# Performance work log

Measured on AMD Instinct MI355X. Metric: run time of the kernel, lower is better.

## Reference

```python
import jax, jax.numpy as jnp
import numpy as np

B, N, M = 8, 1024, 64          # graphs, ops/graph, machines/graph
OPF, MF = 16, 8                # raw feature dims
H, D, L = 8, 64, 3             # heads, head dim, HGT layers
F = H * D                      # 512 = hidden_dim * num_heads
KC = 8                         # compatible machines per op
NOP, NM = B * N, B * M
EPS = 1e-5


def _graph_ln(x, w, b):
    # PyG LayerNorm(mode='graph') with batch=None: scalar mean/std over the whole tensor
    x = x - x.mean()
    return x / (x.std() + EPS) * w + b


def _seg_softmax(a, idx, n):
    amax = jax.ops.segment_max(a, idx, num_segments=n)
    amax = jnp.where(jnp.isfinite(amax), amax, 0.0)
    ex = jnp.exp(a - amax[idx])
    s = jax.ops.segment_sum(ex, idx, num_segments=n)
    return ex / (s[idx] + 1e-16)


def _forward(op_x, machine_x, W_emb_op, b_emb_op, W_emb_m, b_emb_m,
             opn_w, opn_b, mn_w, mn_b, Wk, bk, Wq, bq, Wv, bv,
             A_rel, M_rel, p_rel, W_out, b_out, skip, ln_w, ln_b,
             ei_precedes, ei_canproc, ei_compat):
    x_op = _graph_ln(op_x @ W_emb_op + b_emb_op, opn_w, opn_b)
    x_m = _graph_ln(machine_x @ W_emb_m + b_emb_m, mn_w, mn_b)
    s0, d0 = ei_precedes   # op -> op
    s1, d1 = ei_canproc    # machine -> op
    s2, d2 = ei_compat     # op -> machine
    scale = 1.0 / jnp.sqrt(jnp.float32(D))
    for l in range(L):
        k_op = (x_op @ Wk[l, 0] + bk[l, 0]).reshape(NOP, H, D)
        q_op = (x_op @ Wq[l, 0] + bq[l, 0]).reshape(NOP, H, D)
        v_op = (x_op @ Wv[l, 0] + bv[l, 0]).reshape(NOP, H, D)
        k_m = (x_m @ Wk[l, 1] + bk[l, 1]).reshape(NM, H, D)
        q_m = (x_m @ Wq[l, 1] + bq[l, 1]).reshape(NM, H, D)
        v_m = (x_m @ Wv[l, 1] + bv[l, 1]).reshape(NM, H, D)
        # relation-specific per-head transforms (a_rel/m_rel of HGTConv)
        k0 = jnp.einsum('nhd,hde->nhe', k_op, A_rel[l, 0]); v0 = jnp.einsum('nhd,hde->nhe', v_op, M_rel[l, 0])
        k1 = jnp.einsum('nhd,hde->nhe', k_m, A_rel[l, 1]);  v1 = jnp.einsum('nhd,hde->nhe', v_m, M_rel[l, 1])
        k2 = jnp.einsum('nhd,hde->nhe', k_op, A_rel[l, 2]); v2 = jnp.einsum('nhd,hde->nhe', v_op, M_rel[l, 2])
        # attention into op nodes: joint softmax over both incoming edge types
        a0 = (q_op[d0] * k0[s0]).sum(-1) * p_rel[l, 0] * scale   # [E0,H]
        a1 = (q_op[d1] * k1[s1]).sum(-1) * p_rel[l, 1] * scale   # [E1,H]
        a_op = jnp.concatenate([a0, a1]); dd = jnp.concatenate([d0, d1])
        w = _seg_softmax(a_op, dd, NOP)
        msg = jnp.concatenate([v0[s0], v1[s1]]) * w[:, :, None]
        agg_op = jax.ops.segment_sum(msg, dd, num_segments=NOP).reshape(NOP, F)
        # attention into machine nodes
        a2 = (q_m[d2] * k2[s2]).sum(-1) * p_rel[l, 2] * scale
        w2 = _seg_softmax(a2, d2, NM)
        agg_m = jax.ops.segment_sum(v2[s2] * w2[:, :, None], d2, num_segments=NM).reshape(NM, F)
        # output projection + learned skip gate (HGTConv internals)
        o_op = jax.nn.gelu(agg_op, approximate=False) @ W_out[l, 0] + b_out[l, 0]
        o_m = jax.nn.gelu(agg_m, approximate=False) @ W_out[l, 1] + b_out[l, 1]
        g_op = jax.nn.sigmoid(skip[l, 0]); g_m = jax.nn.sigmoid(skip[l, 1])
        o_op = g_op * o_op + (1.0 - g_op) * x_op
        o_m = g_m * o_m + (1.0 - g_m) * x_m
        # wrapper residual + dropout(eval=identity) + graph layer norm
        x_op = _graph_ln(o_op + x_op, ln_w[l], ln_b[l])
        x_m = _graph_ln(o_m + x_m, ln_w[l], ln_b[l])
    fea_j = x_op.reshape(B, N, F)
    fea_m = x_m.reshape(B, M, F)
    return fea_j, fea_m, fea_j.mean(1, keepdims=True), fea_m.mean(1, keepdims=True)


def setup_inputs() -> dict:
    key = jax.random.key(0)
    ks = jax.random.split(key, 12)
    rng = np.random.default_rng(0)
    ids = np.arange(NOP).reshape(B, N)
    src0 = ids[:, :-1].ravel(); dst0 = ids[:, 1:].ravel()
    mach = rng.integers(0, M, size=(B, N, KC)) + (np.arange(B) * M)[:, None, None]
    ops = np.broadcast_to(ids[:, :, None], (B, N, KC))
    ei_precedes = jnp.asarray(np.stack([src0, dst0]), dtype=jnp.int32)
    ei_canproc = jnp.asarray(np.stack([mach.ravel(), ops.ravel()]), dtype=jnp.int32)
    ei_compat = jnp.asarray(np.stack([ops.ravel(), mach.ravel()]), dtype=jnp.int32)
    n = lambda k, sh, s=0.05: jax.random.normal(k, sh, dtype=jnp.float32) * s
    return dict(
        op_x=n(ks[0], (NOP, OPF), 1.0),
        machine_x=n(ks[1], (NM, MF), 1.0),
        W_emb_op=n(ks[2], (OPF, F)), b_emb_op=jnp.zeros((F,), jnp.float32),
        W_emb_m=n(ks[3], (MF, F)), b_emb_m=jnp.zeros((F,), jnp.float32),
        opn_w=jnp.ones((F,), jnp.float32), opn_b=jnp.zeros((F,), jnp.float32),
        mn_w=jnp.ones((F,), jnp.float32), mn_b=jnp.zeros((F,), jnp.float32),
        Wk=n(ks[4], (L, 2, F, F)), bk=jnp.zeros((L, 2, F), jnp.float32),
        Wq=n(ks[5], (L, 2, F, F)), bq=jnp.zeros((L, 2, F), jnp.float32),
        Wv=n(ks[6], (L, 2, F, F)), bv=jnp.zeros((L, 2, F), jnp.float32),
        A_rel=n(ks[7], (L, 3, H, D, D)), M_rel=n(ks[8], (L, 3, H, D, D)),
        p_rel=jnp.ones((L, 3, H), jnp.float32),
        W_out=n(ks[9], (L, 2, F, F)), b_out=jnp.zeros((L, 2, F), jnp.float32),
        skip=jnp.ones((L, 2), jnp.float32),
        ln_w=jnp.ones((L, F), jnp.float32), ln_b=jnp.zeros((L, F), jnp.float32),
        ei_precedes=ei_precedes, ei_canproc=ei_canproc, ei_compat=ei_compat,
    )


def reference(op_x, machine_x, W_emb_op, b_emb_op, W_emb_m, b_emb_m,
              opn_w, opn_b, mn_w, mn_b, Wk, bk, Wq, bq, Wv, bv,
              A_rel, M_rel, p_rel, W_out, b_out, skip, ln_w, ln_b,
              ei_precedes, ei_canproc, ei_compat):
    return _forward(op_x, machine_x, W_emb_op, b_emb_op, W_emb_m, b_emb_m,
                    opn_w, opn_b, mn_w, mn_b, Wk, bk, Wq, bq, Wv, bv,
                    A_rel, M_rel, p_rel, W_out, b_out, skip, ln_w, ln_b,
                    ei_precedes, ei_canproc, ei_compat)
```

## Files before the change

### kernel.cpp

```cpp
#include <hip/hip_runtime.h>

typedef unsigned short u16;
typedef __attribute__((ext_vector_type(4))) float floatx4;
typedef __attribute__((ext_vector_type(8))) short shortx8;
typedef __attribute__((ext_vector_type(4))) short shortx4;

#define NOPS 8192
#define NMS  512
#define CQ   2560
#define CM   1536
#define TOPC (NOPS*512)
#define TMC  (NMS*512)

__device__ __forceinline__ float bf2f(u16 u){ return __uint_as_float(((unsigned)u)<<16); }
__device__ __forceinline__ u16 f2bf(float f){
  unsigned u = __float_as_uint(f);
  u += 0x7FFFu + ((u>>16)&1u);
  return (u16)(u>>16);
}
__device__ __forceinline__ float wred(float v){
  #pragma unroll
  for (int o=32;o;o>>=1) v += __shfl_xor(v,o,64);
  return v;
}
__device__ __forceinline__ float geluf(float x){
  return 0.5f*x*(1.f+erff(x*0.70710678118654752f));
}
__device__ __forceinline__ void block_stat_out2(float s, float s2, float* pstat, int slot){
  __shared__ float sb[8];
  s = wred(s); s2 = wred(s2);
  int wv = threadIdx.x >> 6;
  if ((threadIdx.x & 63) == 0){ sb[wv*2] = s; sb[wv*2+1] = s2; }
  __syncthreads();
  if (threadIdx.x == 0){
    float a = 0.f, b = 0.f;
    int nw = blockDim.x >> 6;
    for (int i=0;i<nw;++i){ a += sb[i*2]; b += sb[i*2+1]; }
    pstat[slot*2]   = a;
    pstat[slot*2+1] = b;
  }
}

__global__ __launch_bounds__(256) void cnt2_k(const int* __restrict__ s1, float* __restrict__ Ct,
                                              float* __restrict__ Cn){
  int idx = blockIdx.x*256 + threadIdx.x;
  int n = idx >> 6, l = idx & 63;
  const int* row = s1 + n*8;
  int cnt = 0;
  #pragma unroll
  for (int j=0;j<8;++j) cnt += ((row[j] & 63) == l);
  float f = (float)cnt;
  Cn[(size_t)n*64 + l] = f;
  int b = n >> 10, nl = n & 1023;
  Ct[(size_t)((b<<6) + l)*1024 + nl] = f;
}

__global__ __launch_bounds__(256) void tw_k(const float* __restrict__ Wout, const float* __restrict__ Wq,
                                            u16* __restrict__ Wout_t, u16* __restrict__ Wc_op_t,
                                            u16* __restrict__ Wc_m_t){
  __shared__ u16 t[64][65];
  int g = blockIdx.x;
  const float* s; u16* d;
  if (g < 6){
    s = Wout + (size_t)g*262144;
    d = Wout_t + (size_t)g*262144;
  } else {
    int blk = g - 6; int l = blk >> 1, side = blk & 1;
    s = Wq + (size_t)blk*262144;
    d = side ? (Wc_m_t + (size_t)l*CM*512) : (Wc_op_t + (size_t)l*CQ*512);
  }
  int kb = blockIdx.y*64, nb = blockIdx.z*64;
  int tx = threadIdx.x & 63, ty4 = threadIdx.x >> 6;
  #pragma unroll 4
  for (int p=0;p<16;++p){
    int k = ty4 + p*4;
    t[k][tx] = f2bf(s[(size_t)(kb+k)*512 + nb + tx]);
  }
  __syncthreads();
  #pragma unroll 4
  for (int p=0;p<16;++p){
    int n = ty4 + p*4;
    d[(size_t)(nb+n)*512 + kb + tx] = t[tx][n];
  }
}

__global__ void qb_k(const float* __restrict__ bq, float* bias_op, float* bias_m){
  int i = blockIdx.x*blockDim.x + threadIdx.x;
  if (i >= 3072) return;
  int l = i >> 10, side = (i >> 9) & 1, f = i & 511;
  float v = bq[(l*2+side)*512 + f];
  if (side==0) bias_op[l*CQ + f] = v; else bias_m[l*CM + f] = v;
}

__global__ __launch_bounds__(256) void combine3_k(const float* __restrict__ Wk, const float* __restrict__ Wv,
                                                  const float* __restrict__ Ar, const float* __restrict__ Mr,
                                                  u16* __restrict__ Wc_op_t, u16* __restrict__ Wc_m_t){
  __shared__ u16 As[64*72];
  __shared__ u16 Bs[128*72];
  int gx = blockIdx.x;
  int l = gx/48; int rem = gx - l*48; int s = rem >> 3; int h = rem & 7;
  int side = (s < 4) ? 0 : 1;
  int r = (s < 4) ? (s+1) : (s-3);
  int useK = side==0 ? (s==0 || s==2) : (s==4);
  int rel  = side==0 ? ((s<2)?0:2) : 1;
  const float* W   = (useK ? Wk : Wv) + (size_t)(l*2+side)*262144;
  const float* Rel = (useK ? Ar : Mr) + ((size_t)(l*3+rel)*8 + h)*4096;
  int h64 = h*64;
  u16* Wt = side ? (Wc_m_t + (size_t)l*CM*512) : (Wc_op_t + (size_t)l*CQ*512);
  int rbase = r*512 + h64;
  int cc0 = blockIdx.y * 128;
  int tid = threadIdx.x, lane = tid & 63, wave = tid >> 6;
  {
    int d = tid >> 2, e0 = (tid & 3) * 16;
    #pragma unroll
    for (int j=0;j<16;++j) As[(e0+j)*72 + d] = f2bf(Rel[d*64 + e0 + j]);
  }
  {
    int ccl = tid >> 1, d0 = (tid & 1) * 32;
    const float* src = W + (size_t)(cc0+ccl)*512 + h64 + d0;
    #pragma unroll
    for (int j=0;j<32;j+=4){
      floatx4 v = *(const floatx4*)(src + j);
      shortx4 sv;
      #pragma unroll
      for (int e=0;e<4;++e) sv[e] = (short)f2bf(v[e]);
      *(shortx4*)(Bs + ccl*72 + d0 + j) = sv;
    }
  }
  __syncthreads();
  int wm = wave & 1, wn = wave >> 1;
  int mrow = lane & 15, quad = lane >> 4;
  floatx4 acc[2][4];
  #pragma unroll
  for (int a=0;a<2;++a)
    #pragma unroll
    for (int b=0;b<4;++b) acc[a][b] = (floatx4){0.f,0.f,0.f,0.f};
  #pragma unroll
  for (int ks=0; ks<2; ++ks){
    shortx8 af[2], bf[4];
    #pragma unroll
    for (int mt=0;mt<2;++mt) af[mt] = *(const shortx8*)(As + (wm*32 + mt*16 + mrow)*72 + ks*32 + quad*8);
    #pragma unroll
    for (int nt=0;nt<4;++nt) bf[nt] = *(const shortx8*)(Bs + (wn*64 + nt*16 + mrow)*72 + ks*32 + quad*8);
    #pragma unroll
    for (int mt=0;mt<2;++mt)
      #pragma unroll
      for (int nt=0;nt<4;++nt)
        acc[mt][nt] = __builtin_amdgcn_mfma_f32_16x16x32_bf16(af[mt], bf[nt], acc[mt][nt], 0, 0, 0);
  }
  #pragma unroll
  for (int mt=0;mt<2;++mt){
    #pragma unroll
    for (int nt=0;nt<4;++nt){
      int ccl = wn*64 + nt*16 + mrow;
      #pragma unroll
      for (int r2=0;r2<4;++r2){
        int e = wm*32 + mt*16 + quad*4 + r2;
        Wt[(size_t)(rbase + e)*512 + cc0 + ccl] = f2bf(acc[mt][nt][r2]);
      }
    }
  }
}
__global__ void cbias_k(const float* __restrict__ bk, const float* __restrict__ bv,
                        const float* __restrict__ Ar, const float* __restrict__ Mr,
                        float* bias_op, float* bias_m){
  int gx = blockIdx.x; int e = threadIdx.x;
  int l = gx/48; int rem = gx - l*48; int s = rem >> 3; int h = rem & 7;
  int side = (s < 4) ? 0 : 1;
  int r = (s < 4) ? (s+1) : (s-3);
  int useK = side==0 ? (s==0 || s==2) : (s==4);
  int rel  = side==0 ? ((s<2)?0:2) : 1;
  const float* bb  = (useK ? bk : bv) + (size_t)(l*2+side)*512 + h*64;
  const float* Rel = (useK ? Ar : Mr) + ((size_t)(l*3+rel)*8 + h)*4096;
  float acc = 0.f;
  for (int d=0; d<64; ++d) acc += bb[d]*Rel[d*64 + e];
  float* bias = side ? (bias_m + l*CM) : (bias_op + l*CQ);
  bias[r*512 + h*64 + e] = acc;
}

__global__ __launch_bounds__(256) void embed2_k(const float* __restrict__ Xop, const float* __restrict__ Wop,
                                                const float* __restrict__ bop, float* __restrict__ Yop,
                                                const float* __restrict__ Xm, const float* __restrict__ Wm,
                                                const float* __restrict__ bm_, float* __restrict__ Ym,
                                                float* pstat, float* pstat_m){
  int bid = blockIdx.x;
  const float *X, *W, *bias; float *Y, *ps; int K, total, nb, lb;
  if (bid < 1024){ X=Xop; W=Wop; bias=bop; Y=Yop; ps=pstat;   K=16; total=TOPC; nb=1024; lb=bid; }
  else           { X=Xm;  W=Wm;  bias=bm_; Y=Ym;  ps=pstat_m; K=8;  total=TMC;  nb=128;  lb=bid-1024; }
  float s = 0.f, s2 = 0.f;
  for (int idx = lb*256 + threadIdx.x; idx < total; idx += nb*256){
    int n = idx >> 9, f = idx & 511;
    float v = bias[f];
    for (int c=0;c<K;++c) v += X[n*K+c] * W[c*512+f];
    Y[idx] = v;
    s += v; s2 += v*v;
  }
  block_stat_out2(s, s2, ps, lb);
}

__global__ __launch_bounds__(256) void ln2_k(const float* __restrict__ src_op, float* __restrict__ dst_op,
                                             u16* __restrict__ dbf_op, const float* __restrict__ w_op,
                                             const float* __restrict__ b_op,
                                             const float* __restrict__ src_m, float* __restrict__ dst_m,
                                             u16* __restrict__ dbf_m, const float* __restrict__ w_m,
                                             const float* __restrict__ b_m,
                                             const float* __restrict__ pstat, const float* __restrict__ pstat_m,
                                             int nbo, int nbm, int wbf){
  int bid = blockIdx.x;
  const float *src, *w, *b, *ps; float* dst; u16* dbf; int total4, nb, lb, nblk; float inv_n;
  if (bid < 1024){ src=src_op; dst=dst_op; dbf=dbf_op; w=w_op; b=b_op; ps=pstat;
                   total4=TOPC/4; nb=1024; lb=bid; nblk=nbo; inv_n=1.f/TOPC; }
  else           { src=src_m;  dst=dst_m;  dbf=dbf_m;  w=w_m;  b=b_m;  ps=pstat_m;
                   total4=TMC/4;  nb=128;  lb=bid-1024; nblk=nbm; inv_n=1.f/TMC; }
  __shared__ float sb[8];
  __shared__ float mr[2];
  float s = 0.f, s2 = 0.f;
  for (int i = threadIdx.x; i < nblk; i += 256){ s += ps[2*i]; s2 += ps[2*i+1]; }
  s = wred(s); s2 = wred(s2);
  int wv = threadIdx.x >> 6;
  if ((threadIdx.x & 63) == 0){ sb[wv*2] = s; sb[wv*2+1] = s2; }
  __syncthreads();
  if (threadIdx.x == 0){
    float a = 0.f, bsum = 0.f;
    for (int i=0;i<4;++i){ a += sb[i*2]; bsum += sb[i*2+1]; }
    float mean = a * inv_n;
    float var  = fmaxf(bsum * inv_n - mean*mean, 0.f);
    mr[0] = mean;
    mr[1] = 1.f/(sqrtf(var) + 1e-5f);
  }
  __syncthreads();
  float mean = mr[0], rinv = mr[1];
  const floatx4* s4 = (const floatx4*)src;
  floatx4* d4 = (floatx4*)dst;
  shortx4* db4 = (shortx4*)dbf;
  const floatx4* w4 = (const floatx4*)w;
  const floatx4* b4 = (const floatx4*)b;
  for (int i = lb*256 + threadIdx.x; i < total4; i += nb*256){
    int f = i & 127;
    floatx4 v = s4[i], wv2 = w4[f], bv = b4[f];
    shortx4 sv;
    #pragma unroll
    for (int e=0;e<4;++e){ v[e] = (v[e]-mean)*rinv*wv2[e] + bv[e]; sv[e] = (short)f2bf(v[e]); }
    d4[i] = v;
    if (wbf) db4[i] = sv;
  }
}

__device__ __forceinline__ void gemm_gate_core(u16* As, u16* Bs, const u16* __restrict__ A,
                                               const u16* __restrict__ Bt,
                                               const float* __restrict__ xr, const float* __restrict__ bo,
                                               const float* __restrict__ sk, float* __restrict__ Y,
                                               float* pstat, int slot, int bx, int by){
  const int tid = threadIdx.x;
  const int lane = tid & 63, wave = tid >> 6;
  const int bm = by * 128, bn = bx * 128;
  const int wm = wave & 1, wn = wave >> 1;
  const int mrow = lane & 15, quad = lane >> 4;
  const u16* Ab = A + (size_t)bm*512;
  const u16* Bb = Bt + (size_t)bn*512;
  floatx4 acc[4][4];
  #pragma unroll
  for (int a=0;a<4;++a)
    #pragma unroll
    for (int b=0;b<4;++b) acc[a][b] = (floatx4){0.f,0.f,0.f,0.f};
  const int r0 = tid >> 2, c0 = (tid & 3) * 8;
  const int r1 = (tid+256) >> 2, c1 = ((tid+256) & 3) * 8;
  const int lds0 = wave*512;
  const int lds1 = wave*512 + 2048;
  for (int k0 = 0; k0 < 512; k0 += 32){
    __builtin_amdgcn_global_load_lds((const __attribute__((address_space(1))) void*)(Ab + (size_t)r0*512 + k0 + c0),
                                     (__attribute__((address_space(3))) void*)(As + lds0), 16, 0, 0);
    __builtin_amdgcn_global_load_lds((const __attribute__((address_space(1))) void*)(Ab + (size_t)r1*512 + k0 + c1),
                                     (__attribute__((address_space(3))) void*)(As + lds1), 16, 0, 0);
    __builtin_amdgcn_global_load_lds((const __attribute__((address_space(1))) void*)(Bb + (size_t)r0*512 + k0 + c0),
                                     (__attribute__((address_space(3))) void*)(Bs + lds0), 16, 0, 0);
    __builtin_amdgcn_global_load_lds((const __attribute__((address_space(1))) void*)(Bb + (size_t)r1*512 + k0 + c1),
                                     (__attribute__((address_space(3))) void*)(Bs + lds1), 16, 0, 0);
    __syncthreads();
    shortx8 af[4], bf[4];
    #pragma unroll
    for (int mt=0;mt<4;++mt) af[mt] = *(const shortx8*)(As + (wm*64 + mt*16 + mrow)*32 + quad*8);
    #pragma unroll
    for (int nt=0;nt<4;++nt) bf[nt] = *(const shortx8*)(Bs + (wn*64 + nt*16 + mrow)*32 + quad*8);
    #pragma unroll
    for (int mt=0;mt<4;++mt)
      #pragma unroll
      for (int nt=0;nt<4;++nt)
        acc[mt][nt] = __builtin_amdgcn_mfma_f32_16x16x32_bf16(af[mt], bf[nt], acc[mt][nt], 0, 0, 0);
    __syncthreads();
  }
  float g = 1.f/(1.f+expf(-(*sk)));
  float s = 0.f, s2 = 0.f;
  #pragma unroll
  for (int mt=0;mt<4;++mt){
    #pragma unroll
    for (int nt=0;nt<4;++nt){
      int col = bn + wn*64 + nt*16 + mrow;
      float bval = bo[col];
      #pragma unroll
      for (int r2=0;r2<4;++r2){
        int row = bm + wm*64 + mt*16 + quad*4 + r2;
        float v = acc[mt][nt][r2] + bval;
        float o = g*v + (2.f-g)*xr[(size_t)row*512 + col];
        Y[(size_t)row*512 + col] = o;
        s += o; s2 += o*o;
      }
    }
  }
  block_stat_out2(s, s2, pstat, slot);
}
__global__ __launch_bounds__(256) void gemmgate2_k(const u16* A1, const u16* B1, const float* x1,
                                                   const float* bo1, const float* sk1, float* Y1, float* ps1,
                                                   int nblk1,
                                                   const u16* A2, const u16* B2, const float* x2,
                                                   const float* bo2, const float* sk2, float* Y2, float* ps2){
  __shared__ u16 As[128*32];
  __shared__ u16 Bs[128*32];
  int id = blockIdx.x;
  if (id < nblk1) gemm_gate_core(As, Bs, A1, B1, x1, bo1, sk1, Y1, ps1, id, id % 4, id / 4);
  else { int j = id - nblk1; gemm_gate_core(As, Bs, A2, B2, x2, bo2, sk2, Y2, ps2, j, j % 4, j / 4); }
}

__device__ __forceinline__ void stage_half8(const u16* __restrict__ src, int kc, u16* region, int tid){
  int wave = tid >> 6;
  #pragma unroll
  for (int j=0;j<2;++j){
    int idx = j*512 + tid;
    int row = idx >> 2, qp2 = idx & 3;
    int qs = qp2 ^ (((row >> 3) & 1) << 1);
    __builtin_amdgcn_global_load_lds(
      (const __attribute__((address_space(1))) void*)(src + (size_t)row*512 + kc + qs*8),
      (__attribute__((address_space(3))) void*)(region + (j*512 + wave*64)*8),
      16, 0, 0);
  }
}

#define MFMA_QUAD(MH) do { \
  __builtin_amdgcn_s_barrier(); \
  asm volatile("s_waitcnt lgkmcnt(0)" ::: "memory"); \
  __builtin_amdgcn_sched_barrier(0); \
  __builtin_amdgcn_s_setprio(1); \
  _Pragma("unroll") \
  for (int mt=0;mt<4;++mt){ \
    _Pragma("unroll") \
    for (int nt=0;nt<4;++nt) \
      acc[(MH)*4+mt][nt] = __builtin_amdgcn_mfma_f32_16x16x32_bf16(af[mt], bf[nt], acc[(MH)*4+mt][nt], 0, 0, 0); \
  } \
  __builtin_amdgcn_s_setprio(0); \
} while(0)

__global__ __launch_bounds__(512, 2) void gemm8_k(
    const u16* __restrict__ A1, const u16* __restrict__ B1, const float* __restrict__ bias1,
    u16* __restrict__ C1, int N1, int nbx1, int nblk1,
    const u16* __restrict__ A2, const u16* __restrict__ B2, const float* __restrict__ bias2,
    u16* __restrict__ C2, int N2, int nbx2){
  extern __shared__ u16 lds[];
  int id = blockIdx.x;
  const u16 *A, *Bt; const float* bias; u16* C; int N, bx, by;
  if (id < nblk1){
    int xcd = id & 7, loc = id >> 3;
    int wg = xcd * (nblk1 >> 3) + loc;
    A=A1; Bt=B1; bias=bias1; C=C1; N=N1; bx=wg%nbx1; by=wg/nbx1;
  }
  else { int j=id-nblk1; A=A2; Bt=B2; bias=bias2; C=C2; N=N2; bx=j%nbx2; by=j/nbx2; }
  const int tid = threadIdx.x, lane = tid & 63, wave = tid >> 6;
  const int wm = wave & 1, wn = wave >> 1;
  const int mrow = lane & 15, quad = lane >> 4;
  const int qp = quad ^ ((mrow & 8) ? 2 : 0);
  const u16* Ab = A + (size_t)(by*256)*512;
  const u16* Bb = Bt + (size_t)(bx*256)*512;

  floatx4 acc[8][4];
  #pragma unroll
  for (int a=0;a<8;++a)
    #pragma unroll
    for (int b=0;b<4;++b) acc[a][b] = (floatx4){0.f,0.f,0.f,0.f};

  stage_half8(Ab, 0,  lds,          tid);
  stage_half8(Bb, 0,  lds + 16384,  tid);
  stage_half8(Ab, 32, lds + 8192,   tid);
  stage_half8(Bb, 32, lds + 24576,  tid);
  stage_half8(Ab, 64, lds + 32768,  tid);
  stage_half8(Bb, 64, lds + 49152,  tid);
  asm volatile("s_waitcnt vmcnt(8)" ::: "memory");
  __builtin_amdgcn_s_barrier();

  for (int t = 0; t < 8; ++t){
    const int s = t & 1;
    u16* Sbase = lds + s*32768;
    u16* Obase = lds + (s^1)*32768;
    const u16* a0 = Sbase + (wm*128 + mrow)*32 + qp*8;
    const u16* b0 = Sbase + 16384 + (wn*64 + mrow)*32 + qp*8;
    const int kc1 = ((t < 7) ? (t+1) : 7)*64 + 32;
    const int kc2 = ((t < 6) ? (t+2) : 7)*64;
    shortx8 af[4], bf[4];

    #pragma unroll
    for (int mt=0;mt<4;++mt) af[mt] = *(const shortx8*)(a0 + mt*512);
    #pragma unroll
    for (int nt=0;nt<4;++nt) bf[nt] = *(const shortx8*)(b0 + nt*512);
    stage_half8(Ab, kc1, Obase + 8192, tid);
    MFMA_QUAD(0);
    __builtin_amdgcn_s_barrier();

    #pragma unroll
    for (int mt=0;mt<4;++mt) af[mt] = *(const shortx8*)(a0 + 2048 + mt*512);
    stage_half8(Bb, kc1, Obase + 24576, tid);
    MFMA_QUAD(1);
    asm volatile("s_waitcnt vmcnt(8)" ::: "memory");
    __builtin_amdgcn_s_barrier();

    #pragma unroll
    for (int mt=0;mt<4;++mt) af[mt] = *(const shortx8*)(a0 + 8192 + mt*512);
    #pragma unroll
    for (int nt=0;nt<4;++nt) bf[nt] = *(const shortx8*)(b0 + 8192 + nt*512);
    stage_half8(Ab, kc2, Sbase, tid);
    MFMA_QUAD(0);
    __builtin_amdgcn_s_barrier();

    #pragma unroll
    for (int mt=0;mt<4;++mt) af[mt] = *(const shortx8*)(a0 + 8192 + 2048 + mt*512);
    stage_half8(Bb, kc2, Sbase + 16384, tid);
    MFMA_QUAD(1);
    asm volatile("s_waitcnt vmcnt(8)" ::: "memory");
    __builtin_amdgcn_s_barrier();
  }

  const int crow0 = by*256 + wm*128 + quad*4;
  const int ccol0 = bx*256 + wn*64 + mrow;
  float bv[4];
  #pragma unroll
  for (int nt=0;nt<4;++nt) bv[nt] = bias ? bias[ccol0 + nt*16] : 0.f;
  #pragma unroll
  for (int mh=0;mh<2;++mh){
    #pragma unroll
    for (int mt=0;mt<4;++mt){
      int row = crow0 + mh*64 + mt*16;
      #pragma unroll
      for (int nt=0;nt<4;++nt){
        int col = ccol0 + nt*16;
        #pragma unroll
        for (int r2=0;r2<4;++r2)
          C[(size_t)(row+r2)*N + col] = f2bf(acc[mh*4+mt][nt][r2] + bv[nt]);
      }
    }
  }
}

__global__ __launch_bounds__(256) void qk12_k(const u16* __restrict__ qkv_op, const u16* __restrict__ qkv_m,
                                              const float* __restrict__ prel, const float* __restrict__ Cn,
                                              u16* __restrict__ agg_op){
  __shared__ __align__(16) char smem[37376];
  u16* smem16 = (u16*)smem;
  u16* As = smem16;
  u16* Bs = smem16 + 4608;
  float* Sbuf = (float*)smem;
  u16* P   = smem16 + 9216;
  u16* v1T = smem16 + 13824;
  float* wpreS = (float*)(smem + 36864);
  float* linvS = (float*)(smem + 37120);
  int bh = blockIdx.y; int b = bh >> 3, h = bh & 7;
  int n0 = blockIdx.x * 64;
  int tid = threadIdx.x, lane = tid & 63, wave = tid >> 6;
  int mrow = lane & 15, quad = lane >> 4;
  int wm = wave & 1, wn = wave >> 1;
  int srow = tid >> 2, scol = (tid & 3) * 16;
  float p1 = prel[8 + h] * 0.125f;
  {
    const u16* src = qkv_op + (size_t)(b*1024 + n0 + srow)*CQ + h*64 + scol;
    *(shortx8*)(As + srow*72 + scol)     = *(const shortx8*)(src);
    *(shortx8*)(As + srow*72 + scol + 8) = *(const shortx8*)(src + 8);
  }
  {
    const u16* src = qkv_m + (size_t)(b*64 + srow)*CM + 512 + h*64 + scol;
    *(shortx8*)(Bs + srow*72 + scol)     = *(const shortx8*)(src);
    *(shortx8*)(Bs + srow*72 + scol + 8) = *(const shortx8*)(src + 8);
  }
  {
    const u16* src = qkv_m + (size_t)(b*64 + srow)*CM + 1024 + h*64 + scol;
    shortx8 v0 = *(const shortx8*)(src);
    shortx8 v1 = *(const shortx8*)(src + 8);
    #pragma unroll
    for (int e=0;e<8;++e){ v1T[(scol+e)*72 + srow] = (u16)v0[e]; v1T[(scol+8+e)*72 + srow] = (u16)v1[e]; }
  }
  __syncthreads();
  floatx4 acc[2][2];
  #pragma unroll
  for (int a=0;a<2;++a){ acc[a][0] = (floatx4){0,0,0,0}; acc[a][1] = (floatx4){0,0,0,0}; }
  #pragma unroll
  for (int ks=0; ks<2; ++ks){
    shortx8 af[2], bf[2];
    #pragma unroll
    for (int mt=0;mt<2;++mt) af[mt] = *(const shortx8*)(As + (wm*32 + mt*16 + mrow)*72 + ks*32 + quad*8);
    #pragma unroll
    for (int nt=0;nt<2;++nt) bf[nt] = *(const shortx8*)(Bs + (wn*32 + nt*16 + mrow)*72 + ks*32 + quad*8);
    #pragma unroll
    for (int mt=0;mt<2;++mt)
      #pragma unroll
      for (int nt=0;nt<2;++nt)
        acc[mt][nt] = __builtin_amdgcn_mfma_f32_16x16x32_bf16(af[mt], bf[nt], acc[mt][nt], 0, 0, 0);
  }
  __syncthreads();
  #pragma unroll
  for (int mt=0;mt<2;++mt){
    #pragma unroll
    for (int nt=0;nt<2;++nt){
      int m = wn*32 + nt*16 + mrow;
      #pragma unroll
      for (int r2=0;r2<4;++r2){
        int nl = wm*32 + mt*16 + quad*4 + r2;
        Sbuf[nl*66 + m] = acc[mt][nt][r2] * p1;
      }
    }
  }
  __syncthreads();
  {
    int row = srow;
    int mb  = scol;
    int n_g = b*1024 + n0 + row;
    int nl  = n0 + row;
    float sp = -1e30f;
    if (nl > 0){
      float p0 = prel[h] * 0.125f;
      const u16* qp = qkv_op + (size_t)n_g*CQ + h*64 + mb;
      const u16* kp = qkv_op + (size_t)(n_g-1)*CQ + 512 + h*64 + mb;
      shortx8 qa = *(const shortx8*)(qp), qb2 = *(const shortx8*)(qp + 8);
// ... 159 lines not shown
    for (int kk=0; kk<4; ++kk){
      shortx8 af = *(const shortx8*)(Ps + mrow*136 + kk*32 + quad*8);
      shortx8 bf = *(const shortx8*)(vsT + (w*16 + mrow)*136 + kk*32 + quad*8);
      O = __builtin_amdgcn_mfma_f32_16x16x32_bf16(af, bf, O, 0, 0, 0);
    }
    __syncthreads();
  }
  L += __shfl_xor(L, 16, 64);
  L += __shfl_xor(L, 32, 64);
  if (lane < 16) redv[1][w][lane] = L;
  __syncthreads();
  #pragma unroll
  for (int r2=0;r2<4;++r2){
    int m = quad*4 + r2;
    float Ls = redv[1][0][m] + redv[1][1][m] + redv[1][2][m] + redv[1][3][m];
    float v = O[r2] / (Ls + 1e-16f);
    agg_m[(size_t)(b*64 + g*16 + m)*512 + h*64 + w*16 + mrow] = f2bf(geluf(v));
  }
}

__global__ __launch_bounds__(512) void meanj_part_k(const float* __restrict__ xo, float* scratchJ){
  int b = blockIdx.x, chunk = blockIdx.y, f = threadIdx.x;
  float s = 0.f;
  for (int r=0;r<128;++r){
    int row = b*1024 + chunk*128 + r;
    s += xo[(size_t)row*512 + f];
  }
  scratchJ[(b*8 + chunk)*512 + f] = s;
}
__global__ __launch_bounds__(512) void mean2_k(const float* __restrict__ scratchJ, float* __restrict__ out){
  int i = blockIdx.x*512 + threadIdx.x;
  if (i < 4096){
    int b = i >> 9, f = i & 511;
    float s = 0.f;
    #pragma unroll
    for (int c=0;c<8;++c) s += scratchJ[(b*8+c)*512 + f];
    out[4456448 + i] = s * (1.f/1024.f);
  } else {
    int j = i - 4096;
    int b = j >> 9, f = j & 511;
    float s = 0.f;
    for (int r=0;r<64;++r) s += out[(size_t)TOPC + (size_t)(b*64+r)*512 + f];
    out[4460544 + j] = s * (1.f/64.f);
  }
}

extern "C" void kernel_launch(void* const* d_in, const int* in_sizes, int n_in,
                              void* d_out, int out_size, void* d_ws, size_t ws_size,
                              hipStream_t stream){
  const float* op_x      = (const float*)d_in[0];
  const float* machine_x = (const float*)d_in[1];
  const float* W_emb_op  = (const float*)d_in[2];
  const float* b_emb_op  = (const float*)d_in[3];
  const float* W_emb_m   = (const float*)d_in[4];
  const float* b_emb_m   = (const float*)d_in[5];
  const float* opn_w     = (const float*)d_in[6];
  const float* opn_b     = (const float*)d_in[7];
  const float* mn_w      = (const float*)d_in[8];
  const float* mn_b      = (const float*)d_in[9];
  const float* Wk        = (const float*)d_in[10];
  const float* bk        = (const float*)d_in[11];
  const float* Wq        = (const float*)d_in[12];
  const float* bq        = (const float*)d_in[13];
  const float* Wv        = (const float*)d_in[14];
  const float* bv        = (const float*)d_in[15];
  const float* A_rel     = (const float*)d_in[16];
  const float* M_rel     = (const float*)d_in[17];
  const float* p_rel     = (const float*)d_in[18];
  const float* W_out     = (const float*)d_in[19];
  const float* b_out     = (const float*)d_in[20];
  const float* skip      = (const float*)d_in[21];
  const float* ln_w      = (const float*)d_in[22];
  const float* ln_b      = (const float*)d_in[23];
  const int* s1          = (const int*)d_in[25];
  float* out = (float*)d_out;

  char* ws = (char*)d_ws;
  size_t off = 0;
  auto alloc = [&](size_t bytes)->void*{
    void* p = ws + off;
    off = (off + bytes + 255) & ~(size_t)255;
    return p;
  };
  float* pstat     = (float*)alloc(4096*4);
  float* scratchJ  = (float*)alloc(32768*4);
  float* Ct        = (float*)alloc((size_t)NMS*1024*4);
  float* Cn        = (float*)alloc((size_t)NOPS*64*4);
  float* x_op      = (float*)alloc((size_t)NOPS*512*4);
  u16*   x_op_bf   = (u16*)  alloc((size_t)NOPS*512*2);
  float* x_m       = (float*)alloc((size_t)NMS*512*4);
  u16*   x_m_bf    = (u16*)  alloc((size_t)NMS*512*2);
  u16*   qkv_op    = (u16*)  alloc((size_t)NOPS*CQ*2);
  u16*   qkv_m     = (u16*)  alloc((size_t)NMS*CM*2);
  u16*   agg_op    = (u16*)  alloc((size_t)NOPS*512*2);
  u16*   agg_m     = (u16*)  alloc((size_t)NMS*512*2);
  u16*   Wc_op_t   = (u16*)  alloc((size_t)3*CQ*512*2);
  float* bias_op   = (float*)alloc((size_t)3*CQ*4);
  u16*   Wc_m_t    = (u16*)  alloc((size_t)3*CM*512*2);
  float* bias_m    = (float*)alloc((size_t)3*CM*4);
  u16*   Wout_t    = (u16*)  alloc((size_t)6*262144*2);
  float* o_op      = (float*)qkv_op;
  float* o_m       = (float*)qkv_m;
  float* pstat_m   = pstat + 2048;

  cnt2_k<<<2048,256,0,stream>>>(s1, Ct, Cn);
  tw_k<<<dim3(12,8,8),256,0,stream>>>(W_out, Wq, Wout_t, Wc_op_t, Wc_m_t);
  qb_k<<<12,256,0,stream>>>(bq, bias_op, bias_m);
  combine3_k<<<dim3(144,4),256,0,stream>>>(Wk, Wv, A_rel, M_rel, Wc_op_t, Wc_m_t);
  cbias_k<<<144,64,0,stream>>>(bk, bv, A_rel, M_rel, bias_op, bias_m);

  embed2_k<<<1152,256,0,stream>>>(op_x, W_emb_op, b_emb_op, x_op,
                                  machine_x, W_emb_m, b_emb_m, x_m, pstat, pstat_m);
  ln2_k<<<1152,256,0,stream>>>(x_op, x_op, x_op_bf, opn_w, opn_b,
                               x_m, x_m, x_m_bf, mn_w, mn_b, pstat, pstat_m, 1024, 128, 1);

  for (int l=0; l<3; ++l){
    int last = (l == 2);
    gemm8_k<<<332,512,131072,stream>>>(x_op_bf, Wc_op_t + (size_t)l*CQ*512, bias_op + l*CQ, qkv_op, CQ, 10, 320,
                                       x_m_bf, Wc_m_t + (size_t)l*CM*512, bias_m + l*CM, qkv_m, CM, 6);
    qk12_k<<<dim3(16,64),256,0,stream>>>(qkv_op, qkv_m, p_rel + l*24, Cn, agg_op);
    mattn_k<<<dim3(4,64),256,0,stream>>>(qkv_op, qkv_m, p_rel + l*24, Ct, agg_m);
    gemmgate2_k<<<272,256,0,stream>>>(agg_op, Wout_t + (size_t)(l*2+0)*262144, x_op,
                                      b_out + (size_t)(l*2+0)*512, skip + l*2+0, o_op, pstat, 256,
                                      agg_m, Wout_t + (size_t)(l*2+1)*262144, x_m,
                                      b_out + (size_t)(l*2+1)*512, skip + l*2+1, o_m, pstat_m);
    ln2_k<<<1152,256,0,stream>>>(o_op, last ? out : x_op, x_op_bf, ln_w + l*512, ln_b + l*512,
                                 o_m, last ? (out + TOPC) : x_m, x_m_bf, ln_w + l*512, ln_b + l*512,
                                 pstat, pstat_m, 256, 16, last ? 0 : 1);
  }

  meanj_part_k<<<dim3(8,8),512,0,stream>>>(out, scratchJ);
  mean2_k<<<16,512,0,stream>>>(scratchJ, out);
}
```

Baseline: 574.2 us.

## Fold graph LayerNorm into QKV GEMM weights and fuse residual normalization

Folds each scalar-statistics graph LayerNorm into the next layer's projection. The LN weight is pre-multiplied into the combined QKV weights, and per-column vectors u and bias corrections are precomputed. The GEMM then applies mean and rstd, reduced from partial stats at block start, in its epilogue, and the gate GEMM normalizes the residual on the fly and writes the bf16 copy directly. This removes the per-layer standalone LN pass and its full-tensor read/write, and merges the small setup kernels into one launch. The GEMM now consumes un-normalized activations in bf16, which may cost some accuracy.

```diff
diff --git a/kernel.cpp b/kernel.cpp
--- a/kernel.cpp
+++ b/kernel.cpp
@@ -41,18 +41,43 @@
   }
 }
 
-__global__ __launch_bounds__(256) void cnt2_k(const int* __restrict__ s1, float* __restrict__ Ct,
-                                              float* __restrict__ Cn){
-  int idx = blockIdx.x*256 + threadIdx.x;
-  int n = idx >> 6, l = idx & 63;
-  const int* row = s1 + n*8;
-  int cnt = 0;
-  #pragma unroll
-  for (int j=0;j<8;++j) cnt += ((row[j] & 63) == l);
-  float f = (float)cnt;
-  Cn[(size_t)n*64 + l] = f;
-  int b = n >> 10, nl = n & 1023;
-  Ct[(size_t)((b<<6) + l)*1024 + nl] = f;
+__global__ __launch_bounds__(256) void setup1_k(const int* __restrict__ s1, float* __restrict__ Ct,
+                                                float* __restrict__ Cn,
+                                                const float* __restrict__ bq, float* bias_op, float* bias_m,
+                                                const float* __restrict__ bk, const float* __restrict__ bv,
+                                                const float* __restrict__ Ar, const float* __restrict__ Mr){
+  int bid = blockIdx.x;
+  if (bid < 2048){
+    int idx = bid*256 + threadIdx.x;
+    int n = idx >> 6, l = idx & 63;
+    const int* row = s1 + n*8;
+    int cnt = 0;
+    #pragma unroll
+    for (int j=0;j<8;++j) cnt += ((row[j] & 63) == l);
+    float f = (float)cnt;
+    Cn[(size_t)n*64 + l] = f;
+    int b = n >> 10, nl = n & 1023;
+    Ct[(size_t)((b<<6) + l)*1024 + nl] = f;
+  } else if (bid < 2060){
+    int i = (bid-2048)*256 + threadIdx.x;
+    int l = i >> 10, side = (i >> 9) & 1, f = i & 511;
+    float v = bq[(l*2+side)*512 + f];
+    if (side==0) bias_op[l*CQ + f] = v; else bias_m[l*CM + f] = v;
+  } else {
+    if (threadIdx.x >= 64) return;
+    int gx = bid - 2060; int e = threadIdx.x;
+    int l = gx/48; int rem = gx - l*48; int s = rem >> 3; int h = rem & 7;
+    int side = (s < 4) ? 0 : 1;
+    int r = (s < 4) ? (s+1) : (s-3);
+    int useK = side==0 ? (s==0 || s==2) : (s==4);
+    int rel  = side==0 ? ((s<2)?0:2) : 1;
+    const float* bb  = (useK ? bk : bv) + (size_t)(l*2+side)*512 + h*64;
+    const float* Rel = (useK ? Ar : Mr) + ((size_t)(l*3+rel)*8 + h)*4096;
+    float acc = 0.f;
+    for (int d=0; d<64; ++d) acc += bb[d]*Rel[d*64 + e];
+    float* bias = side ? (bias_m + l*CM) : (bias_op + l*CQ);
+    bias[r*512 + h*64 + e] = acc;
+  }
 }
 
 __global__ __launch_bounds__(256) void tw_k(const float* __restrict__ Wout, const float* __restrict__ Wq,
@@ -82,14 +107,6 @@
     int n = ty4 + p*4;
     d[(size_t)(nb+n)*512 + kb + tx] = t[tx][n];
   }
-}
-
-__global__ void qb_k(const float* __restrict__ bq, float* bias_op, float* bias_m){
-  int i = blockIdx.x*blockDim.x + threadIdx.x;
-  if (i >= 3072) return;
-  int l = i >> 10, side = (i >> 9) & 1, f = i & 511;
-  float v = bq[(l*2+side)*512 + f];
-  if (side==0) bias_op[l*CQ + f] = v; else bias_m[l*CM + f] = v;
 }
 
 __global__ __launch_bounds__(256) void combine3_k(const float* __restrict__ Wk, const float* __restrict__ Wv,
@@ -161,56 +178,76 @@
     }
   }
 }
-__global__ void cbias_k(const float* __restrict__ bk, const float* __restrict__ bv,
-                        const float* __restrict__ Ar, const float* __restrict__ Mr,
-                        float* bias_op, float* bias_m){
-  int gx = blockIdx.x; int e = threadIdx.x;
-  int l = gx/48; int rem = gx - l*48; int s = rem >> 3; int h = rem & 7;
-  int side = (s < 4) ? 0 : 1;
-  int r = (s < 4) ? (s+1) : (s-3);
-  int useK = side==0 ? (s==0 || s==2) : (s==4);
-  int rel  = side==0 ? ((s<2)?0:2) : 1;
-  const float* bb  = (useK ? bk : bv) + (size_t)(l*2+side)*512 + h*64;
-  const float* Rel = (useK ? Ar : Mr) + ((size_t)(l*3+rel)*8 + h)*4096;
-  float acc = 0.f;
-  for (int d=0; d<64; ++d) acc += bb[d]*Rel[d*64 + e];
-  float* bias = side ? (bias_m + l*CM) : (bias_op + l*CQ);
-  bias[r*512 + h*64 + e] = acc;
+
+__global__ __launch_bounds__(256) void foldk(u16* __restrict__ Wc_op_t, u16* __restrict__ Wc_m_t,
+                                             float* __restrict__ bias_op, float* __restrict__ bias_m,
+                                             float* __restrict__ u_op, float* __restrict__ u_m,
+                                             const float* __restrict__ opn_w, const float* __restrict__ opn_b,
+                                             const float* __restrict__ mn_w, const float* __restrict__ mn_b,
+                                             const float* __restrict__ ln_w, const float* __restrict__ ln_b){
+  int bid = blockIdx.x, tid = threadIdx.x;
+  int rloc = tid >> 2, t = tid & 3;
+  int side, l; u16* Wt; float* bias; float* u;
+  if (bid < 120){
+    int row = bid*64 + rloc; side = 0; l = row/2560; int j = row - l*2560;
+    Wt = Wc_op_t + ((size_t)l*CQ + j)*512; bias = bias_op + l*CQ + j; u = u_op + l*CQ + j;
+  } else {
+    int row = (bid-120)*64 + rloc; side = 1; l = row/1536; int j = row - l*1536;
+    Wt = Wc_m_t + ((size_t)l*CM + j)*512; bias = bias_m + l*CM + j; u = u_m + l*CM + j;
+  }
+  const float* w = side ? (l==0 ? mn_w : ln_w + (l-1)*512) : (l==0 ? opn_w : ln_w + (l-1)*512);
+  const float* b = side ? (l==0 ? mn_b : ln_b + (l-1)*512) : (l==0 ? opn_b : ln_b + (l-1)*512);
+  float up = 0.f, vp = 0.f;
+  for (int k = t*128; k < t*128 + 128; k += 8){
+    shortx8 wv = *(shortx8*)(Wt + k);
+    #pragma unroll
+    for (int e=0;e<8;++e){
+      float x = bf2f((u16)wv[e]);
+      float wk = w[k+e];
+      up += wk*x; vp += b[k+e]*x;
+      wv[e] = (short)f2bf(x*wk);
+    }
+    *(shortx8*)(Wt + k) = wv;
+  }
+  up += __shfl_xor(up,1,64); up += __shfl_xor(up,2,64);
+  vp += __shfl_xor(vp,1,64); vp += __shfl_xor(vp,2,64);
+  if (t == 0){ *u = up; *bias += vp; }
 }
 
 __global__ __launch_bounds__(256) void embed2_k(const float* __restrict__ Xop, const float* __restrict__ Wop,
                                                 const float* __restrict__ bop, float* __restrict__ Yop,
+                                                u16* __restrict__ Yop_bf,
                                                 const float* __restrict__ Xm, const float* __restrict__ Wm,
                                                 const float* __restrict__ bm_, float* __restrict__ Ym,
+                                                u16* __restrict__ Ym_bf,
                                                 float* pstat, float* pstat_m){
   int bid = blockIdx.x;
-  const float *X, *W, *bias; float *Y, *ps; int K, total, nb, lb;
-  if (bid < 1024){ X=Xop; W=Wop; bias=bop; Y=Yop; ps=pstat;   K=16; total=TOPC; nb=1024; lb=bid; }
-  else           { X=Xm;  W=Wm;  bias=bm_; Y=Ym;  ps=pstat_m; K=8;  total=TMC;  nb=128;  lb=bid-1024; }
+  const float *X, *W, *bias; float *Y, *ps; u16* Yb; int K, total, nb, lb;
+  if (bid < 1024){ X=Xop; W=Wop; bias=bop; Y=Yop; Yb=Yop_bf; ps=pstat;   K=16; total=TOPC; nb=1024; lb=bid; }
+  else           { X=Xm;  W=Wm;  bias=bm_; Y=Ym;  Yb=Ym_bf;  ps=pstat_m; K=8;  total=TMC;  nb=128;  lb=bid-1024; }
   float s = 0.f, s2 = 0.f;
   for (int idx = lb*256 + threadIdx.x; idx < total; idx += nb*256){
     int n = idx >> 9, f = idx & 511;
     float v = bias[f];
     for (int c=0;c<K;++c) v += X[n*K+c] * W[c*512+f];
     Y[idx] = v;
+    Yb[idx] = f2bf(v);
     s += v; s2 += v*v;
   }
   block_stat_out2(s, s2, ps, lb);
 }
 
 __global__ __launch_bounds__(256) void ln2_k(const float* __restrict__ src_op, float* __restrict__ dst_op,
-                                             u16* __restrict__ dbf_op, const float* __restrict__ w_op,
-                                             const float* __restrict__ b_op,
+                                             const float* __restrict__ w_op, const float* __restrict__ b_op,
                                              const float* __restrict__ src_m, float* __restrict__ dst_m,
-                                             u16* __restrict__ dbf_m, const float* __restrict__ w_m,
-                                             const float* __restrict__ b_m,
+                                             const float* __restrict__ w_m, const float* __restrict__ b_m,
                                              const float* __restrict__ pstat, const float* __restrict__ pstat_m,
-                                             int nbo, int nbm, int wbf){
+                                             int nbo, int nbm){
   int bid = blockIdx.x;
-  const float *src, *w, *b, *ps; float* dst; u16* dbf; int total4, nb, lb, nblk; float inv_n;
-  if (bid < 1024){ src=src_op; dst=dst_op; dbf=dbf_op; w=w_op; b=b_op; ps=pstat;
+  const float *src, *w, *b, *ps; float* dst; int total4, nb, lb, nblk; float inv_n;
+  if (bid < 1024){ src=src_op; dst=dst_op; w=w_op; b=b_op; ps=pstat;
                    total4=TOPC/4; nb=1024; lb=bid; nblk=nbo; inv_n=1.f/TOPC; }
-  else           { src=src_m;  dst=dst_m;  dbf=dbf_m;  w=w_m;  b=b_m;  ps=pstat_m;
+  else           { src=src_m;  dst=dst_m;  w=w_m;  b=b_m;  ps=pstat_m;
                    total4=TMC/4;  nb=128;  lb=bid-1024; nblk=nbm; inv_n=1.f/TMC; }
   __shared__ float sb[8];
   __shared__ float mr[2];
@@ -232,27 +269,44 @@
   float mean = mr[0], rinv = mr[1];
   const floatx4* s4 = (const floatx4*)src;
   floatx4* d4 = (floatx4*)dst;
-  shortx4* db4 = (shortx4*)dbf;
   const floatx4* w4 = (const floatx4*)w;
   const floatx4* b4 = (const floatx4*)b;
   for (int i = lb*256 + threadIdx.x; i < total4; i += nb*256){
     int f = i & 127;
     floatx4 v = s4[i], wv2 = w4[f], bv = b4[f];
-    shortx4 sv;
-    #pragma unroll
-    for (int e=0;e<4;++e){ v[e] = (v[e]-mean)*rinv*wv2[e] + bv[e]; sv[e] = (short)f2bf(v[e]); }
+    #pragma unroll
+    for (int e=0;e<4;++e) v[e] = (v[e]-mean)*rinv*wv2[e] + bv[e];
     d4[i] = v;
-    if (wbf) db4[i] = sv;
-  }
-}
-
-__device__ __forceinline__ void gemm_gate_core(u16* As, u16* Bs, const u16* __restrict__ A,
-                                               const u16* __restrict__ Bt,
+  }
+}
+
+__device__ __forceinline__ void gemm_gate_core(u16* As, u16* Bs, float* stb,
+                                               const u16* __restrict__ A, const u16* __restrict__ Bt,
                                                const float* __restrict__ xr, const float* __restrict__ bo,
-                                               const float* __restrict__ sk, float* __restrict__ Y,
+                                               const float* __restrict__ sk,
+                                               const float* __restrict__ lnw, const float* __restrict__ lnb,
+                                               const float* __restrict__ psr, int np, float inv_n,
+                                               float* __restrict__ Y, u16* __restrict__ Ybf,
                                                float* pstat, int slot, int bx, int by){
   const int tid = threadIdx.x;
   const int lane = tid & 63, wave = tid >> 6;
+  {
+    float s = 0.f, s2 = 0.f;
+    for (int i = tid; i < np; i += 256){ s += psr[2*i]; s2 += psr[2*i+1]; }
+    s = wred(s); s2 = wred(s2);
+    if (lane == 0){ stb[wave*2] = s; stb[wave*2+1] = s2; }
+    __syncthreads();
+    if (tid == 0){
+      float a = 0.f, bb = 0.f;
+      for (int i=0;i<4;++i){ a += stb[2*i]; bb += stb[2*i+1]; }
+      float mean = a * inv_n;
+      float var = fmaxf(bb * inv_n - mean*mean, 0.f);
+      stb[8] = mean;
+      stb[9] = 1.f/(sqrtf(var) + 1e-5f);
+    }
+    __syncthreads();
+  }
+  const float mean = stb[8], rinv = stb[9];
   const int bm = by * 128, bn = bx * 128;
   const int wm = wave & 1, wn = wave >> 1;
   const int mrow = lane & 15, quad = lane >> 4;
@@ -297,28 +351,39 @@
     for (int nt=0;nt<4;++nt){
       int col = bn + wn*64 + nt*16 + mrow;
       float bval = bo[col];
+      float lw = lnw[col]*rinv, lb = lnb[col];
       #pragma unroll
       for (int r2=0;r2<4;++r2){
         int row = bm + wm*64 + mt*16 + quad*4 + r2;
         float v = acc[mt][nt][r2] + bval;
-        float o = g*v + (2.f-g)*xr[(size_t)row*512 + col];
+        float xv = (xr[(size_t)row*512 + col] - mean)*lw + lb;
+        float o = g*v + (2.f-g)*xv;
         Y[(size_t)row*512 + col] = o;
+        Ybf[(size_t)row*512 + col] = f2bf(o);
         s += o; s2 += o*o;
       }
     }
   }
   block_stat_out2(s, s2, pstat, slot);
 }
-__global__ __launch_bounds__(256) void gemmgate2_k(const u16* A1, const u16* B1, const float* x1,
-                                                   const float* bo1, const float* sk1, float* Y1, float* ps1,
-                                                   int nblk1,
-                                                   const u16* A2, const u16* B2, const float* x2,
-                                                   const float* bo2, const float* sk2, float* Y2, float* ps2){
+__global__ __launch_bounds__(256) void gemmgate2_k(
+    const u16* A1, const u16* B1, const float* x1, const float* bo1, const float* sk1,
+    const float* lnw1, const float* lnb1, float* Y1, u16* Yb1, float* ps1w, int nblk1,
+    const u16* A2, const u16* B2, const float* x2, const float* bo2, const float* sk2,
+    const float* lnw2, const float* lnb2, float* Y2, u16* Yb2, float* ps2w,
+    const float* ps1r, int np1, const float* ps2r, int np2){
   __shared__ u16 As[128*32];
   __shared__ u16 Bs[128*32];
+  __shared__ float stb[12];
   int id = blockIdx.x;
-  if (id < nblk1) gemm_gate_core(As, Bs, A1, B1, x1, bo1, sk1, Y1, ps1, id, id % 4, id / 4);
-  else { int j = id - nblk1; gemm_gate_core(As, Bs, A2, B2, x2, bo2, sk2, Y2, ps2, j, j % 4, j / 4); }
+  if (id < nblk1)
+    gemm_gate_core(As, Bs, stb, A1, B1, x1, bo1, sk1, lnw1, lnb1, ps1r, np1, 1.f/TOPC,
+                   Y1, Yb1, ps1w, id, id % 4, id / 4);
+  else {
+    int j = id - nblk1;
+    gemm_gate_core(As, Bs, stb, A2, B2, x2, bo2, sk2, lnw2, lnb2, ps2r, np2, 1.f/TMC,
+                   Y2, Yb2, ps2w, j, j % 4, j / 4);
+  }
 }
 
 __device__ __forceinline__ void stage_half8(const u16* __restrict__ src, int kc, u16* region, int tid){
@@ -351,19 +416,40 @@
 
 __global__ __launch_bounds__(512, 2) void gemm8_k(
     const u16* __restrict__ A1, const u16* __restrict__ B1, const float* __restrict__ bias1,
-    u16* __restrict__ C1, int N1, int nbx1, int nblk1,
-    const u16* __restrict__ A2, const u16* __restrict__ B2, const float* __restrict__ bias2,
-    u16* __restrict__ C2, int N2, int nbx2){
+    const float* __restrict__ u1, u16* __restrict__ C1, int N1, int nbx1, int nblk1,
+    const u16* __restrict__ A2, const u16* __restrict__ B2, const float* __restrict__ bias2p,
+    const float* __restrict__ u2, u16* __restrict__ C2, int N2, int nbx2,
+    const float* __restrict__ ps1, int np1, const float* __restrict__ ps2, int np2){
   extern __shared__ u16 lds[];
+  float* statsh = (float*)(lds + 65536);
   int id = blockIdx.x;
-  const u16 *A, *Bt; const float* bias; u16* C; int N, bx, by;
+  const u16 *A, *Bt; const float *bias, *uvec, *ps; u16* C; int N, bx, by, np; float inv_n;
   if (id < nblk1){
     int xcd = id & 7, loc = id >> 3;
     int wg = xcd * (nblk1 >> 3) + loc;
-    A=A1; Bt=B1; bias=bias1; C=C1; N=N1; bx=wg%nbx1; by=wg/nbx1;
-  }
-  else { int j=id-nblk1; A=A2; Bt=B2; bias=bias2; C=C2; N=N2; bx=j%nbx2; by=j/nbx2; }
+    A=A1; Bt=B1; bias=bias1; uvec=u1; C=C1; N=N1; bx=wg%nbx1; by=wg/nbx1;
+    ps=ps1; np=np1; inv_n=1.f/TOPC;
+  }
+  else { int j=id-nblk1; A=A2; Bt=B2; bias=bias2p; uvec=u2; C=C2; N=N2; bx=j%nbx2; by=j/nbx2;
+    ps=ps2; np=np2; inv_n=1.f/TMC; }
   const int tid = threadIdx.x, lane = tid & 63, wave = tid >> 6;
+  {
+    float s = 0.f, s2 = 0.f;
+    for (int i = tid; i < np; i += 512){ s += ps[2*i]; s2 += ps[2*i+1]; }
+    s = wred(s); s2 = wred(s2);
+    if (lane == 0){ statsh[wave*2] = s; statsh[wave*2+1] = s2; }
+    __syncthreads();
+    if (tid == 0){
+      float a = 0.f, bb = 0.f;
+      for (int i=0;i<8;++i){ a += statsh[2*i]; bb += statsh[2*i+1]; }
+      float mean = a * inv_n;
+      float var = fmaxf(bb * inv_n - mean*mean, 0.f);
+      statsh[16] = mean;
+      statsh[17] = 1.f/(sqrtf(var) + 1e-5f);
+    }
+    __syncthreads();
+  }
+  const float mean = statsh[16], rinv = statsh[17];
   const int wm = wave & 1, wn = wave >> 1;
   const int mrow = lane & 15, quad = lane >> 4;
   const int qp = quad ^ ((mrow & 8) ? 2 : 0);
@@ -426,11 +512,16 @@
     __builtin_amdgcn_s_barrier();
   }
 
+  const float rm = rinv*mean;
   const int crow0 = by*256 + wm*128 + quad*4;
   const int ccol0 = bx*256 + wn*64 + mrow;
-  float bv[4];
-  #pragma unroll
-  for (int nt=0;nt<4;++nt) bv[nt] = bias ? bias[ccol0 + nt*16] : 0.f;
+  float bv[4], uv[4];
+  #pragma unroll
+  for (int nt=0;nt<4;++nt){
+    int col = ccol0 + nt*16;
+    bv[nt] = bias[col];
+    uv[nt] = uvec[col];
+  }
   #pragma unroll
   for (int mh=0;mh<2;++mh){
     #pragma unroll
@@ -441,7 +532,7 @@
         int col = ccol0 + nt*16;
         #pragma unroll
         for (int r2=0;r2<4;++r2)
-          C[(size_t)(row+r2)*N + col] = f2bf(acc[mh*4+mt][nt][r2] + bv[nt]);
+          C[(size_t)(row+r2)*N + col] = f2bf(rinv*acc[mh*4+mt][nt][r2] + bv[nt] - rm*uv[nt]);
       }
     }
   }
@@ -767,7 +858,7 @@
     off = (off + bytes + 255) & ~(size_t)255;
     return p;
   };
-  float* pstat     = (float*)alloc(4096*4);
+  float* pstat     = (float*)alloc(8192*4);
   float* scratchJ  = (float*)alloc(32768*4);
   float* Ct        = (float*)alloc((size_t)NMS*1024*4);
   float* Cn        = (float*)alloc((size_t)NOPS*64*4);
@@ -783,36 +874,49 @@
   float* bias_op   = (float*)alloc((size_t)3*CQ*4);
   u16*   Wc_m_t    = (u16*)  alloc((size_t)3*CM*512*2);
   float* bias_m    = (float*)alloc((size_t)3*CM*4);
+  float* u_op      = (float*)alloc((size_t)3*CQ*4);
+  float* u_m       = (float*)alloc((size_t)3*CM*4);
   u16*   Wout_t    = (u16*)  alloc((size_t)6*262144*2);
-  float* o_op      = (float*)qkv_op;
-  float* o_m       = (float*)qkv_m;
-  float* pstat_m   = pstat + 2048;
-
-  cnt2_k<<<2048,256,0,stream>>>(s1, Ct, Cn);
+  float* psA   = pstat;          float* psA_m = pstat + 2048;
+  float* psB   = pstat + 4096;   float* psB_m = pstat + 6144;
+
+  setup1_k<<<2204,256,0,stream>>>(s1, Ct, Cn, bq, bias_op, bias_m, bk, bv, A_rel, M_rel);
   tw_k<<<dim3(12,8,8),256,0,stream>>>(W_out, Wq, Wout_t, Wc_op_t, Wc_m_t);
-  qb_k<<<12,256,0,stream>>>(bq, bias_op, bias_m);
   combine3_k<<<dim3(144,4),256,0,stream>>>(Wk, Wv, A_rel, M_rel, Wc_op_t, Wc_m_t);
-  cbias_k<<<144,64,0,stream>>>(bk, bv, A_rel, M_rel, bias_op, bias_m);
-
-  embed2_k<<<1152,256,0,stream>>>(op_x, W_emb_op, b_emb_op, x_op,
-                                  machine_x, W_emb_m, b_emb_m, x_m, pstat, pstat_m);
-  ln2_k<<<1152,256,0,stream>>>(x_op, x_op, x_op_bf, opn_w, opn_b,
-                               x_m, x_m, x_m_bf, mn_w, mn_b, pstat, pstat_m, 1024, 128, 1);
+  foldk<<<192,256,0,stream>>>(Wc_op_t, Wc_m_t, bias_op, bias_m, u_op, u_m,
+                              opn_w, opn_b, mn_w, mn_b, ln_w, ln_b);
+
+  embed2_k<<<1152,256,0,stream>>>(op_x, W_emb_op, b_emb_op, x_op, x_op_bf,
+                                  machine_x, W_emb_m, b_emb_m, x_m, x_m_bf, psA, psA_m);
 
   for (int l=0; l<3; ++l){
-    int last = (l == 2);
-    gemm8_k<<<332,512,131072,stream>>>(x_op_bf, Wc_op_t + (size_t)l*CQ*512, bias_op + l*CQ, qkv_op, CQ, 10, 320,
-                                       x_m_bf, Wc_m_t + (size_t)l*CM*512, bias_m + l*CM, qkv_m, CM, 6);
+    float *psR, *psR_m, *psW, *psW_m; int npo, npm;
+    if (l == 0){ psR=psA; psR_m=psA_m; psW=psB; psW_m=psB_m; npo=1024; npm=128; }
+    else if (l == 1){ psR=psB; psR_m=psB_m; psW=psA; psW_m=psA_m; npo=256; npm=16; }
+    else { psR=psA; psR_m=psA_m; psW=psB; psW_m=psB_m; npo=256; npm=16; }
+    const float* lnw_o = (l==0) ? opn_w : ln_w + (l-1)*512;
+    const float* lnb_o = (l==0) ? opn_b : ln_b + (l-1)*512;
+    const float* lnw_m2 = (l==0) ? mn_w : ln_w + (l-1)*512;
+    const float* lnb_m2 = (l==0) ? mn_b : ln_b + (l-1)*512;
+    gemm8_k<<<332,512,131136,stream>>>(x_op_bf, Wc_op_t + (size_t)l*CQ*512, bias_op + l*CQ, u_op + l*CQ,
+                                       qkv_op, CQ, 10, 320,
+                                       x_m_bf, Wc_m_t + (size_t)l*CM*512, bias_m + l*CM, u_m + l*CM,
+                                       qkv_m, CM, 6,
+                                       psR, npo, psR_m, npm);
     qk12_k<<<dim3(16,64),256,0,stream>>>(qkv_op, qkv_m, p_rel + l*24, Cn, agg_op);
     mattn_k<<<dim3(4,64),256,0,stream>>>(qkv_op, qkv_m, p_rel + l*24, Ct, agg_m);
     gemmgate2_k<<<272,256,0,stream>>>(agg_op, Wout_t + (size_t)(l*2+0)*262144, x_op,
-                                      b_out + (size_t)(l*2+0)*512, skip + l*2+0, o_op, pstat, 256,
+                                      b_out + (size_t)(l*2+0)*512, skip + l*2+0,
+                                      lnw_o, lnb_o, x_op, x_op_bf, psW, 256,
                                       agg_m, Wout_t + (size_t)(l*2+1)*262144, x_m,
-                                      b_out + (size_t)(l*2+1)*512, skip + l*2+1, o_m, pstat_m);
-    ln2_k<<<1152,256,0,stream>>>(o_op, last ? out : x_op, x_op_bf, ln_w + l*512, ln_b + l*512,
-                                 o_m, last ? (out + TOPC) : x_m, x_m_bf, ln_w + l*512, ln_b + l*512,
-                                 pstat, pstat_m, 256, 16, last ? 0 : 1);
-  }
+                                      b_out + (size_t)(l*2+1)*512, skip + l*2+1,
+                                      lnw_m2, lnb_m2, x_m, x_m_bf, psW_m,
+                                      psR, npo, psR_m, npm);
+  }
+
+  ln2_k<<<1152,256,0,stream>>>(x_op, out, ln_w + 1024, ln_b + 1024,
+                               x_m, out + TOPC, ln_w + 1024, ln_b + 1024,
+                               psB, psB_m, 256, 16);
 
   meanj_part_k<<<dim3(8,8),512,0,stream>>>(out, scratchJ);
   mean2_k<<<16,512,0,stream>>>(scratchJ, out);
```

New measurement: 575.1 us. Within noise of the previous version (+0.2%).
